# Optimization experiments

Hardware: AMD Instinct MI355X
Metric: run time of the kernel (lower is better)

Reference implementation:

```python
import jax, jax.numpy as jnp
import numpy as np

NEG_SLOPE = 0.2
EPS = 1e-16

N_NODES = 50000
N_EDGES = 1600000
IN_CH = 256
HID = 16
HEADS = 2


def setup_inputs() -> dict:
    key = jax.random.key(0)
    ks = jax.random.split(key, 12)
    s = lambda k, shape, scale=0.1: jax.random.normal(k, shape, dtype=jnp.float32) * scale
    x = jax.random.normal(ks[0], (N_NODES, IN_CH), dtype=jnp.float32)
    edge_index = jax.random.randint(ks[1], (2, N_EDGES), 0, N_NODES, dtype=jnp.int64)
    return {
        "x": x,
        "edge_index": edge_index,
        "W1": s(ks[2], (IN_CH, HEADS * HID)),
        "att_src1": s(ks[3], (HEADS, HID)),
        "att_dst1": s(ks[4], (HEADS, HID)),
        "b1": jnp.zeros((HEADS * HID,), jnp.float32),
        "W2": s(ks[5], (HEADS * HID, HID)),
        "att_src2": s(ks[6], (1, HID)),
        "att_dst2": s(ks[7], (1, HID)),
        "b2": jnp.zeros((HID,), jnp.float32),
        "Wm1": s(ks[8], (2 * HID, HID)),
        "bm1": jnp.zeros((HID,), jnp.float32),
        "Wm2": s(ks[9], (HID, 1)),
        "bm2": jnp.zeros((1,), jnp.float32),
    }


def gat_conv(x, src, dst, W, att_src, att_dst, bias, heads, out_ch, concat):
    # x: [N, F] -> h: [N, H, C]
    n = x.shape[0]
    h = (x @ W).reshape(n, heads, out_ch)
    # per-node attention logits [N, H]
    a_src = jnp.sum(h * att_src, axis=-1)
    a_dst = jnp.sum(h * att_dst, axis=-1)
    # per-edge logits: message j (src) -> i (dst); softmax grouped by dst
    e = a_src[src] + a_dst[dst]                      # [E, H]
    e = jax.nn.leaky_relu(e, NEG_SLOPE)
    e_max = jax.ops.segment_max(e, dst, num_segments=n)
    e_exp = jnp.exp(e - e_max[dst])
    denom = jax.ops.segment_sum(e_exp, dst, num_segments=n)
    alpha = e_exp / (denom[dst] + EPS)               # [E, H]
    msg = alpha[:, :, None] * h[src]                 # [E, H, C]
    out = jax.ops.segment_sum(msg, dst, num_segments=n)  # [N, H, C]
    out = out.reshape(n, heads * out_ch) if concat else out.mean(axis=1)
    return out + bias


def reference(x, edge_index, W1, att_src1, att_dst1, b1,
              W2, att_src2, att_dst2, b2, Wm1, bm1, Wm2, bm2):
    src, dst = edge_index[0], edge_index[1]
    # eval mode: feature/attention dropout are identity
    h = gat_conv(x, src, dst, W1, att_src1, att_dst1, b1, HEADS, HID, concat=True)
    h = jax.nn.elu(h)
    h = gat_conv(h, src, dst, W2, att_src2, att_dst2, b2, 1, HID, concat=False)
    # edge MLP on gathered (src, dst) node pairs
    ef = jnp.concatenate([h[src], h[dst]], axis=-1)  # [E, 2*HID]
    ef = jax.nn.relu(ef @ Wm1 + bm1)
    flow = (ef @ Wm2 + bm2).squeeze(-1)              # [E]
    return jax.nn.relu(flow)
```

## Files before the change

### kernel.cpp

```cpp
#include <hip/hip_runtime.h>
#include <hip/hip_bf16.h>
#include <hip/hip_fp16.h>

#define N_NODES 50000
#define N_EDGES 1600000
#define IN_CH 256
#define NEG_SLOPE 0.2f
#define EPS_F 1e-16f
#define CNT_PAD 16
#define CAP 128
#define NBK 196
#define CAPB 10240
#define PCHUNK 3125
#define KTILE 128
#define XS_PITCH (KTILE + 4)

__device__ __forceinline__ float lrelu(float x) {
    return x > 0.f ? x : NEG_SLOPE * x;
}

__device__ __forceinline__ float2 h2f(unsigned int w) {
    __half2 h;
    *reinterpret_cast<unsigned int*>(&h) = w;
    return __half22float2(h);
}

__device__ __forceinline__ unsigned int f2h2(float a, float b) {
    __half2 h = __floats2half2_rn(a, b);
    return *reinterpret_cast<unsigned int*>(&h);
}

__global__ __launch_bounds__(256) void k0_detect(const int* __restrict__ ei,
                                                 int* __restrict__ flag,
                                                 int* __restrict__ gcnt)
{
    __shared__ int nz;
    const int t = threadIdx.x;
    if (t == 0) nz = 0;
    if (t < 256) gcnt[t] = 0;
    __syncthreads();
    if (t & 1) { if (ei[t] != 0) atomicAdd(&nz, 1); }
    __syncthreads();
    if (t == 0) flag[0] = (nz == 0) ? 1 : 0;
}

__device__ __forceinline__ int ld_src(const int* ei, int f, int e) {
    return f ? ei[2 * (size_t)e] : ei[e];
}
__device__ __forceinline__ int ld_dst(const int* ei, int f, int e) {
    return f ? ei[2 * (size_t)N_EDGES + 2 * (size_t)e]
             : ei[(size_t)N_EDGES + e];
}

__global__ __launch_bounds__(1024) void k_part(const int* __restrict__ ei,
                                               const int* __restrict__ flag,
                                               int* __restrict__ gcnt,
                                               int2* __restrict__ bseg)
{
    __shared__ int hist[NBK];
    __shared__ int cur[NBK];
    const int t = threadIdx.x;
    for (int j = t; j < NBK; j += 1024) hist[j] = 0;
    __syncthreads();
    const int f = flag[0];
    const int e0 = blockIdx.x * PCHUNK;
    const int e1 = min(e0 + PCHUNK, N_EDGES);
    for (int e = e0 + t; e < e1; e += 1024)
        atomicAdd(&hist[ld_dst(ei, f, e) >> 8], 1);
    __syncthreads();
    for (int j = t; j < NBK; j += 1024)
        cur[j] = j * CAPB + atomicAdd(&gcnt[j], hist[j]);
    __syncthreads();
    for (int e = e0 + t; e < e1; e += 1024) {
        const int s = ld_src(ei, f, e);
        const int d = ld_dst(ei, f, e);
        const int bk = d >> 8;
        const int pos = atomicAdd(&cur[bk], 1);
        if (pos - bk * CAPB < CAPB) bseg[pos] = make_int2(s, d);
    }
}

__global__ __launch_bounds__(1024) void k_sub(const int* __restrict__ gcnt,
                                              const int2* __restrict__ bseg,
                                              int* __restrict__ cnt,
                                              int* __restrict__ csr_src)
{
    __shared__ int cur[256];
    const int b = blockIdx.x;
    const int t = threadIdx.x;
    if (t < 256) cur[t] = 0;
    __syncthreads();
    const int count = min(gcnt[b], CAPB);
    const int2* seg = bseg + (size_t)b * CAPB;
    for (int i = t; i < count; i += 1024) {
        const int2 e = seg[i];
        const int slot = atomicAdd(&cur[e.y & 255], 1);
        if (slot < CAP) csr_src[((size_t)e.y << 7) + slot] = e.x;
    }
    __syncthreads();
    if (t < 256) {
        const int n = b * 256 + t;
        if (n < N_NODES) cnt[(size_t)n * CNT_PAD] = min(cur[t], CAP);
    }
}

__global__ __launch_bounds__(256) void k1_gemm1(
    const float* __restrict__ x, const float* __restrict__ W1,
    const float* __restrict__ att_src1, const float* __restrict__ att_dst1,
    __half* __restrict__ h1, float* __restrict__ a_src1, float* __restrict__ a_dst1)
{
    __shared__ float w1s[IN_CH * 32];
    __shared__ float xs[64 * XS_PITCH];
    __shared__ float attss[32], attds[32];
    const int t = threadIdx.x;
    for (int i = t; i < IN_CH * 32; i += 256) w1s[i] = W1[i];
    if (t < 32) { attss[t] = att_src1[t]; attds[t] = att_dst1[t]; }
    const int row0 = blockIdx.x * 64;
    const int colq = t & 7, c4 = colq * 4;
    const int rp = t >> 3;
    const int r0 = rp * 2, r1 = r0 + 1;
    float4 a0 = make_float4(0.f, 0.f, 0.f, 0.f);
    float4 a1 = make_float4(0.f, 0.f, 0.f, 0.f);
    for (int kb = 0; kb < IN_CH; kb += KTILE) {
        __syncthreads();
        #pragma unroll
        for (int i = 0; i < 8; ++i) {
            const int idx = t + 256 * i;
            const int r = idx >> 5, p = idx & 31;
            const int row = row0 + r;
            float4 vv = make_float4(0.f, 0.f, 0.f, 0.f);
            if (row < N_NODES)
                vv = *(const float4*)(x + (size_t)row * IN_CH + kb + p * 4);
            *(float4*)(&xs[r * XS_PITCH + p * 4]) = vv;
        }
        __syncthreads();
        #pragma unroll 8
        for (int kt = 0; kt < KTILE; ++kt) {
            const float xv0 = xs[r0 * XS_PITCH + kt];
            const float xv1 = xs[r1 * XS_PITCH + kt];
            const float4 wv = *(const float4*)(&w1s[(kb + kt) * 32 + c4]);
            a0.x += xv0 * wv.x; a0.y += xv0 * wv.y;
            a0.z += xv0 * wv.z; a0.w += xv0 * wv.w;
            a1.x += xv1 * wv.x; a1.y += xv1 * wv.y;
            a1.z += xv1 * wv.z; a1.w += xv1 * wv.w;
        }
    }
    const int row_a = row0 + r0, row_b = row0 + r1;
    if (row_a < N_NODES) {
        uint2 p; p.x = f2h2(a0.x, a0.y); p.y = f2h2(a0.z, a0.w);
        *(uint2*)(h1 + (size_t)row_a * 32 + c4) = p;
    }
    if (row_b < N_NODES) {
        uint2 p; p.x = f2h2(a1.x, a1.y); p.y = f2h2(a1.z, a1.w);
        *(uint2*)(h1 + (size_t)row_b * 32 + c4) = p;
    }
    float sa0 = a0.x * attss[c4] + a0.y * attss[c4 + 1]
              + a0.z * attss[c4 + 2] + a0.w * attss[c4 + 3];
    float sd0 = a0.x * attds[c4] + a0.y * attds[c4 + 1]
              + a0.z * attds[c4 + 2] + a0.w * attds[c4 + 3];
    float sa1 = a1.x * attss[c4] + a1.y * attss[c4 + 1]
              + a1.z * attss[c4 + 2] + a1.w * attss[c4 + 3];
    float sd1 = a1.x * attds[c4] + a1.y * attds[c4 + 1]
              + a1.z * attds[c4 + 2] + a1.w * attds[c4 + 3];
    sa0 += __shfl_xor(sa0, 1); sa0 += __shfl_xor(sa0, 2);
    sd0 += __shfl_xor(sd0, 1); sd0 += __shfl_xor(sd0, 2);
    sa1 += __shfl_xor(sa1, 1); sa1 += __shfl_xor(sa1, 2);
    sd1 += __shfl_xor(sd1, 1); sd1 += __shfl_xor(sd1, 2);
    const int head = colq >> 2;
    if ((colq & 3) == 0) {
        if (row_a < N_NODES) {
            a_src1[row_a * 2 + head] = sa0;
            a_dst1[row_a * 2 + head] = sd0;
        }
        if (row_b < N_NODES) {
            a_src1[row_b * 2 + head] = sa1;
            a_dst1[row_b * 2 + head] = sd1;
        }
    }
}

__global__ __launch_bounds__(256) void k_agg1(
    const int* __restrict__ cnt, const int* __restrict__ csr_src,
    const float* __restrict__ a_src1, const float* __restrict__ a_dst1,
    const __half* __restrict__ h1, float* __restrict__ out1)
{
    const int wid = (blockIdx.x * 256 + threadIdx.x) >> 6;
    const int lane = threadIdx.x & 63;
    if (wid >= N_NODES) return;
    const int len = min(cnt[(size_t)wid * CNT_PAD], CAP);
    const int beg = wid << 7, end = beg + len;
    const float2 ad = *(const float2*)(a_dst1 + 2 * (size_t)wid);
    const int slot = lane >> 5, ch = lane & 31;
    const int head = ch >> 4;
    const float adh = head ? ad.y : ad.x;
    const int rep = ((ch & 15) == 0);
    float acc = 0.f, sw = 0.f;
    int i = beg + slot;
    for (; i + 14 < end; i += 16) {
        int s[8]; float a[8], h[8], w[8];
        #pragma unroll
        for (int j = 0; j < 8; ++j) s[j] = csr_src[i + 2 * j];
        #pragma unroll
        for (int j = 0; j < 8; ++j) a[j] = a_src1[2 * (size_t)s[j] + head];
        #pragma unroll
        for (int j = 0; j < 8; ++j) h[j] = __half2float(h1[(size_t)s[j] * 32 + ch]);
        #pragma unroll
        for (int j = 0; j < 8; ++j) w[j] = __expf(lrelu(a[j] + adh));
        float wsum = 0.f;
        #pragma unroll
        for (int j = 0; j < 8; ++j) { wsum += w[j]; acc += w[j] * h[j]; }
        if (rep) sw += wsum;
    }
    for (; i < end; i += 2) {
        const int s = csr_src[i];
        const float w = __expf(lrelu(a_src1[2 * (size_t)s + head] + adh));
        if (rep) sw += w;
        acc += w * __half2float(h1[(size_t)s * 32 + ch]);
    }
    sw += __shfl_xor(sw, 32);
    const float swh = __shfl(sw, head << 4);
    acc += __shfl_xor(acc, 32);
    const float inv = 1.f / (swh + EPS_F);
    if (lane < 32) out1[(size_t)wid * 32 + lane] = acc * inv;
}

__global__ __launch_bounds__(256) void k4_layer2(
    const float* __restrict__ out1, const float* __restrict__ b1,
    const float* __restrict__ W2, const float* __restrict__ att_src2,
    const float* __restrict__ att_dst2,
    float* __restrict__ h2, float* __restrict__ a_src2, float* __restrict__ a_dst2)
{
    __shared__ float act[16][32];
    __shared__ float w2s[32 * 16];
    __shared__ float b1s[32], as2[16], ad2[16];
    const int t = threadIdx.x;
    for (int i = t; i < 512; i += 256) w2s[i] = W2[i];
    if (t < 32) b1s[t] = b1[t];
    if (t < 16) { as2[t] = att_src2[t]; ad2[t] = att_dst2[t]; }
    __syncthreads();
    const int node0 = blockIdx.x * 16;
    for (int i = t; i < 512; i += 256) {
        const int nl = i >> 5, k = i & 31;
        const int row = node0 + nl;
        float v = 0.f;
        if (row < N_NODES) {
            v = out1[(size_t)row * 32 + k] + b1s[k];
            v = v > 0.f ? v : expm1f(v);
        }
        act[nl][k] = v;
    }
    __syncthreads();
    const int nl = t >> 4, j = t & 15;
    const int row = node0 + nl;
    float acc = 0.f;
    #pragma unroll
    for (int k = 0; k < 32; ++k) acc += act[nl][k] * w2s[k * 16 + j];
    if (row < N_NODES) h2[(size_t)row * 16 + j] = acc;
    float sa = acc * as2[j], sd = acc * ad2[j];
    #pragma unroll
    for (int m = 1; m < 16; m <<= 1) { sa += __shfl_xor(sa, m); sd += __shfl_xor(sd, m); }
    if (j == 0 && row < N_NODES) { a_src2[row] = sa; a_dst2[row] = sd; }
}

__global__ __launch_bounds__(256) void k_agg2(
    const int* __restrict__ cnt, const int* __restrict__ csr_src,
    const float* __restrict__ a_src2, const float* __restrict__ a_dst2,
    const float* __restrict__ h2, float* __restrict__ out2)
{
    const int wid = (blockIdx.x * 256 + threadIdx.x) >> 6;
    const int lane = threadIdx.x & 63;
    if (wid >= N_NODES) return;
    const int len = min(cnt[(size_t)wid * CNT_PAD], CAP);
    const int beg = wid << 7, end = beg + len;
    const float ad = a_dst2[wid];
    const int slot = lane >> 4, ch = lane & 15;
    const int rep = (ch == 0);
    float acc = 0.f, sw = 0.f;
    int i = beg + slot;
    for (; i + 28 < end; i += 32) {
        int s[8]; float a[8], h[8], w[8];
        #pragma unroll
        for (int j = 0; j < 8; ++j) s[j] = csr_src[i + 4 * j];
        #pragma unroll
        for (int j = 0; j < 8; ++j) a[j] = a_src2[s[j]];
        #pragma unroll
        for (int j = 0; j < 8; ++j) h[j] = h2[(size_t)s[j] * 16 + ch];
        #pragma unroll
        for (int j = 0; j < 8; ++j) w[j] = __expf(lrelu(a[j] + ad));
        float wsum = 0.f;
        #pragma unroll
        for (int j = 0; j < 8; ++j) { wsum += w[j]; acc += w[j] * h[j]; }
        if (rep) sw += wsum;
    }
    for (; i < end; i += 4) {
        const int s = csr_src[i];
        const float w = __expf(lrelu(a_src2[s] + ad));
        if (rep) sw += w;
        acc += w * h2[(size_t)s * 16 + ch];
    }
    #pragma unroll
    for (int m = 1; m < 64; m <<= 1) sw += __shfl_xor(sw, m);
    acc += __shfl_xor(acc, 16);
    acc += __shfl_xor(acc, 32);
    const float inv = 1.f / (sw + EPS_F);
    if (lane < 16) out2[(size_t)wid * 16 + lane] = acc * inv;
}

__global__ __launch_bounds__(256) void k_prep(
    const float* __restrict__ out2, const float* __restrict__ b2,
    const float* __restrict__ Wm1, const float* __restrict__ bm1,
    __half* __restrict__ u, __half* __restrict__ v)
{
    __shared__ float wa[16 * 16], wb[16 * 16];
    __shared__ float act[16][17];
    __shared__ float b2s[16], bm1s[16];
    const int t = threadIdx.x;
    if (t < 256) {
        const int k = t >> 4, j = t & 15;
        wa[t] = Wm1[k * 16 + j];
        wb[t] = Wm1[(16 + k) * 16 + j];
    }
    if (t < 16) { b2s[t] = b2[t]; bm1s[t] = bm1[t]; }
    __syncthreads();
    const int node0 = blockIdx.x * 16;
    const int nl = t >> 4, c = t & 15;
    const int row = node0 + nl;
    act[nl][c] = (row < N_NODES) ? out2[(size_t)row * 16 + c] + b2s[c] : 0.f;
    __syncthreads();
    float su = bm1s[c], sv = 0.f;
    #pragma unroll
    for (int k = 0; k < 16; ++k) {
        const float a = act[nl][k];
        su += a * wa[k * 16 + c];
        sv += a * wb[k * 16 + c];
    }
    if (row < N_NODES) {
        u[(size_t)row * 16 + c] = __float2half(su);
        v[(size_t)row * 16 + c] = __float2half(sv);
    }
}

__global__ __launch_bounds__(256) void k7_lite(
    const int* __restrict__ ei, const int* __restrict__ flag,
    const __half* __restrict__ u, const __half* __restrict__ v,
    const float* __restrict__ Wm2, const float* __restrict__ bm2,
    float* __restrict__ out)
{
    __shared__ float wm2s[16];
    __shared__ float bm2s;
    const int t = threadIdx.x;
    if (t < 16) wm2s[t] = Wm2[t];
    if (t == 0) bm2s = bm2[0];
    __syncthreads();
    const int e = blockIdx.x * 256 + t;
    if (e >= N_EDGES) return;
    const int f = flag[0];
    const int s = ld_src(ei, f, e);
    const int d = ld_dst(ei, f, e);
    const uint4* up = (const uint4*)(u + (size_t)s * 16);
    const uint4* vp = (const uint4*)(v + (size_t)d * 16);
    const uint4 ua = up[0], ub = up[1];
    const uint4 va = vp[0], vb = vp[1];
    float fl = bm2s;
    unsigned int uw[8] = {ua.x, ua.y, ua.z, ua.w, ub.x, ub.y, ub.z, ub.w};
    unsigned int vw[8] = {va.x, va.y, va.z, va.w, vb.x, vb.y, vb.z, vb.w};
    #pragma unroll
    for (int i = 0; i < 8; ++i) {
        const float2 a = h2f(uw[i]);
        const float2 b = h2f(vw[i]);
        fl += fmaxf(a.x + b.x, 0.f) * wm2s[2 * i];
        fl += fmaxf(a.y + b.y, 0.f) * wm2s[2 * i + 1];
    }
    out[e] = fmaxf(fl, 0.f);
}

extern "C" void kernel_launch(void* const* d_in, const int* in_sizes, int n_in,
                              void* d_out, int out_size, void* d_ws, size_t ws_size,
                              hipStream_t stream)
{
    const float* x        = (const float*)d_in[0];
    const int*   ei       = (const int*)d_in[1];
    const float* W1       = (const float*)d_in[2];
    const float* att_src1 = (const float*)d_in[3];
    const float* att_dst1 = (const float*)d_in[4];
    const float* b1       = (const float*)d_in[5];
    const float* W2       = (const float*)d_in[6];
    const float* att_src2 = (const float*)d_in[7];
    const float* att_dst2 = (const float*)d_in[8];
    const float* b2       = (const float*)d_in[9];
    const float* Wm1      = (const float*)d_in[10];
    const float* bm1      = (const float*)d_in[11];
    const float* Wm2      = (const float*)d_in[12];
    const float* bm2      = (const float*)d_in[13];

    float* ws = (float*)d_ws;
    size_t off = 0;
    __half* h1 = (__half*)(ws + off); off += 16 * (size_t)N_NODES;
    float* a_src1 = ws + off; off += 2  * (size_t)N_NODES;
    float* a_dst1 = ws + off; off += 2  * (size_t)N_NODES;
    float* out1   = ws + off; off += 32 * (size_t)N_NODES;
    float* h2     = ws + off; off += 16 * (size_t)N_NODES;
    float* a_src2 = ws + off; off += 1  * (size_t)N_NODES;
    float* a_dst2 = ws + off; off += 1  * (size_t)N_NODES;
    float* out2   = ws + off; off += 16 * (size_t)N_NODES;
    __half* u = (__half*)(ws + off); off += 8 * (size_t)N_NODES;
    __half* v = (__half*)(ws + off); off += 8 * (size_t)N_NODES;
    int* cnt     = (int*)(ws + off); off += (size_t)N_NODES * CNT_PAD;
    int* csr_src = (int*)(ws + off); off += (size_t)N_NODES * CAP;
    int* gcnt    = (int*)(ws + off); off += 256;
    int* flag    = (int*)(ws + off); off += 64;
    int2* bseg = (int2*)ws;

    k0_detect<<<1, 256, 0, stream>>>(ei, flag, gcnt);
    k_part<<<(N_EDGES + PCHUNK - 1) / PCHUNK, 1024, 0, stream>>>(ei, flag, gcnt, bseg);
    k_sub<<<NBK, 1024, 0, stream>>>(gcnt, bseg, cnt, csr_src);

    k1_gemm1<<<(N_NODES + 63) / 64, 256, 0, stream>>>(
        x, W1, att_src1, att_dst1, h1, a_src1, a_dst1);
    k_agg1<<<(N_NODES + 3) / 4, 256, 0, stream>>>(
        cnt, csr_src, a_src1, a_dst1, h1, out1);
    k4_layer2<<<(N_NODES + 15) / 16, 256, 0, stream>>>(
        out1, b1, W2, att_src2, att_dst2, h2, a_src2, a_dst2);
    k_agg2<<<(N_NODES + 3) / 4, 256, 0, stream>>>(
        cnt, csr_src, a_src2, a_dst2, h2, out2);
    k_prep<<<(N_NODES + 15) / 16, 256, 0, stream>>>(
        out2, b2, Wm1, bm1, u, v);
    k7_lite<<<(N_EDGES + 255) / 256, 256, 0, stream>>>(
        ei, flag, u, v, Wm2, bm2, (float*)d_out);
}
```

Baseline: 280.5 us.

## Precompute per-edge attention weights in separate kernels before aggregation

Adds two kernels that compute exp(leaky_relu(a_src+a_dst)) once per CSR edge slot and store them in padded per-node weight arrays. The aggregation kernels then read these weights instead of gathering a_src and recomputing the exponent, which had been redundant across the 32 or 16 channel lanes. This costs two extra launches and extra global writes and reads of the weight buffers (grids cover N*CAP slots, most of them idle). It also halves the GEMM K tile, which shrinks shared memory.

```diff
diff --git a/kernel.cpp b/kernel.cpp
--- a/kernel.cpp
+++ b/kernel.cpp
@@ -12,7 +12,7 @@
 #define NBK 196
 #define CAPB 10240
 #define PCHUNK 3125
-#define KTILE 128
+#define KTILE 64
 #define XS_PITCH (KTILE + 4)
 
 __device__ __forceinline__ float lrelu(float x) {
@@ -124,9 +124,9 @@
     for (int kb = 0; kb < IN_CH; kb += KTILE) {
         __syncthreads();
         #pragma unroll
-        for (int i = 0; i < 8; ++i) {
+        for (int i = 0; i < 4; ++i) {
             const int idx = t + 256 * i;
-            const int r = idx >> 5, p = idx & 31;
+            const int r = idx >> 4, p = idx & 15;
             const int row = row0 + r;
             float4 vv = make_float4(0.f, 0.f, 0.f, 0.f);
             if (row < N_NODES)
@@ -179,9 +179,25 @@
     }
 }
 
+__global__ __launch_bounds__(256) void k_wgt1(
+    const int* __restrict__ cnt, const int* __restrict__ csr_src,
+    const float* __restrict__ a_src1, const float* __restrict__ a_dst1,
+    float2* __restrict__ wgt1)
+{
+    const int idx = blockIdx.x * 256 + threadIdx.x;
+    const int n = idx >> 7, slot = idx & 127;
+    if (n >= N_NODES) return;
+    if (slot >= cnt[(size_t)n * CNT_PAD]) return;
+    const int s = csr_src[idx];
+    const float2 as = *(const float2*)(a_src1 + 2 * (size_t)s);
+    const float2 ad = *(const float2*)(a_dst1 + 2 * (size_t)n);
+    wgt1[idx] = make_float2(__expf(lrelu(as.x + ad.x)),
+                            __expf(lrelu(as.y + ad.y)));
+}
+
 __global__ __launch_bounds__(256) void k_agg1(
     const int* __restrict__ cnt, const int* __restrict__ csr_src,
-    const float* __restrict__ a_src1, const float* __restrict__ a_dst1,
+    const float* __restrict__ wgtf,
     const __half* __restrict__ h1, float* __restrict__ out1)
 {
     const int wid = (blockIdx.x * 256 + threadIdx.x) >> 6;
@@ -189,23 +205,19 @@
     if (wid >= N_NODES) return;
     const int len = min(cnt[(size_t)wid * CNT_PAD], CAP);
     const int beg = wid << 7, end = beg + len;
-    const float2 ad = *(const float2*)(a_dst1 + 2 * (size_t)wid);
     const int slot = lane >> 5, ch = lane & 31;
     const int head = ch >> 4;
-    const float adh = head ? ad.y : ad.x;
     const int rep = ((ch & 15) == 0);
     float acc = 0.f, sw = 0.f;
     int i = beg + slot;
     for (; i + 14 < end; i += 16) {
-        int s[8]; float a[8], h[8], w[8];
+        int s[8]; float w[8], h[8];
         #pragma unroll
         for (int j = 0; j < 8; ++j) s[j] = csr_src[i + 2 * j];
         #pragma unroll
-        for (int j = 0; j < 8; ++j) a[j] = a_src1[2 * (size_t)s[j] + head];
+        for (int j = 0; j < 8; ++j) w[j] = wgtf[2 * (size_t)(i + 2 * j) + head];
         #pragma unroll
         for (int j = 0; j < 8; ++j) h[j] = __half2float(h1[(size_t)s[j] * 32 + ch]);
-        #pragma unroll
-        for (int j = 0; j < 8; ++j) w[j] = __expf(lrelu(a[j] + adh));
         float wsum = 0.f;
         #pragma unroll
         for (int j = 0; j < 8; ++j) { wsum += w[j]; acc += w[j] * h[j]; }
@@ -213,7 +225,7 @@
     }
     for (; i < end; i += 2) {
         const int s = csr_src[i];
-        const float w = __expf(lrelu(a_src1[2 * (size_t)s + head] + adh));
+        const float w = wgtf[2 * (size_t)i + head];
         if (rep) sw += w;
         acc += w * __half2float(h1[(size_t)s * 32 + ch]);
     }
@@ -262,9 +274,22 @@
     if (j == 0 && row < N_NODES) { a_src2[row] = sa; a_dst2[row] = sd; }
 }
 
+__global__ __launch_bounds__(256) void k_wgt2(
+    const int* __restrict__ cnt, const int* __restrict__ csr_src,
+    const float* __restrict__ a_src2, const float* __restrict__ a_dst2,
+    float* __restrict__ wgt2)
+{
+    const int idx = blockIdx.x * 256 + threadIdx.x;
+    const int n = idx >> 7, slot = idx & 127;
+    if (n >= N_NODES) return;
+    if (slot >= cnt[(size_t)n * CNT_PAD]) return;
+    const int s = csr_src[idx];
+    wgt2[idx] = __expf(lrelu(a_src2[s] + a_dst2[n]));
+}
+
 __global__ __launch_bounds__(256) void k_agg2(
     const int* __restrict__ cnt, const int* __restrict__ csr_src,
-    const float* __restrict__ a_src2, const float* __restrict__ a_dst2,
+    const float* __restrict__ wgt2,
     const float* __restrict__ h2, float* __restrict__ out2)
 {
     const int wid = (blockIdx.x * 256 + threadIdx.x) >> 6;
@@ -272,21 +297,18 @@
     if (wid >= N_NODES) return;
     const int len = min(cnt[(size_t)wid * CNT_PAD], CAP);
     const int beg = wid << 7, end = beg + len;
-    const float ad = a_dst2[wid];
     const int slot = lane >> 4, ch = lane & 15;
     const int rep = (ch == 0);
     float acc = 0.f, sw = 0.f;
     int i = beg + slot;
     for (; i + 28 < end; i += 32) {
-        int s[8]; float a[8], h[8], w[8];
+        int s[8]; float w[8], h[8];
         #pragma unroll
         for (int j = 0; j < 8; ++j) s[j] = csr_src[i + 4 * j];
         #pragma unroll
-        for (int j = 0; j < 8; ++j) a[j] = a_src2[s[j]];
+        for (int j = 0; j < 8; ++j) w[j] = wgt2[i + 4 * j];
         #pragma unroll
         for (int j = 0; j < 8; ++j) h[j] = h2[(size_t)s[j] * 16 + ch];
-        #pragma unroll
-        for (int j = 0; j < 8; ++j) w[j] = __expf(lrelu(a[j] + ad));
         float wsum = 0.f;
         #pragma unroll
         for (int j = 0; j < 8; ++j) { wsum += w[j]; acc += w[j] * h[j]; }
@@ -294,7 +316,7 @@
     }
     for (; i < end; i += 4) {
         const int s = csr_src[i];
-        const float w = __expf(lrelu(a_src2[s] + ad));
+        const float w = wgt2[i];
         if (rep) sw += w;
         acc += w * h2[(size_t)s * 16 + ch];
     }
@@ -407,6 +429,8 @@
     __half* v = (__half*)(ws + off); off += 8 * (size_t)N_NODES;
     int* cnt     = (int*)(ws + off); off += (size_t)N_NODES * CNT_PAD;
     int* csr_src = (int*)(ws + off); off += (size_t)N_NODES * CAP;
+    float2* wgt1 = (float2*)(ws + off); off += 2 * (size_t)N_NODES * CAP;
+    float* wgt2  = ws + off; off += (size_t)N_NODES * CAP;
     int* gcnt    = (int*)(ws + off); off += 256;
     int* flag    = (int*)(ws + off); off += 64;
     int2* bseg = (int2*)ws;
@@ -417,12 +441,16 @@
 
     k1_gemm1<<<(N_NODES + 63) / 64, 256, 0, stream>>>(
         x, W1, att_src1, att_dst1, h1, a_src1, a_dst1);
+    k_wgt1<<<(N_NODES * CAP + 255) / 256, 256, 0, stream>>>(
+        cnt, csr_src, a_src1, a_dst1, wgt1);
     k_agg1<<<(N_NODES + 3) / 4, 256, 0, stream>>>(
-        cnt, csr_src, a_src1, a_dst1, h1, out1);
+        cnt, csr_src, (const float*)wgt1, h1, out1);
     k4_layer2<<<(N_NODES + 15) / 16, 256, 0, stream>>>(
         out1, b1, W2, att_src2, att_dst2, h2, a_src2, a_dst2);
+    k_wgt2<<<(N_NODES * CAP + 255) / 256, 256, 0, stream>>>(
+        cnt, csr_src, a_src2, a_dst2, wgt2);
     k_agg2<<<(N_NODES + 3) / 4, 256, 0, stream>>>(
-        cnt, csr_src, a_src2, a_dst2, h2, out2);
+        cnt, csr_src, wgt2, h2, out2);
     k_prep<<<(N_NODES + 15) / 16, 256, 0, stream>>>(
         out2, b2, Wm1, bm1, u, v);
     k7_lite<<<(N_EDGES + 255) / 256, 256, 0, stream>>>(
```

Result: slower. 306.9 us (+9.4%).
